# Optimization experiments

Hardware: AMD Instinct MI355X
Metric: run time of the kernel (lower is better)

The kernel has to match this reference:

```python
import jax, jax.numpy as jnp
import numpy as np

N_NODES = 50000
N_EDGES = 600000
IN_DIM = 128
HID = 128
FEAT = 128
N_TASKS = 5
N_CLS = 10


def setup_inputs() -> dict:
    key = jax.random.key(0)
    ks = jax.random.split(key, 10)
    s = 0.05  # small init scale for weights
    return {
        "x": jax.random.normal(ks[0], (N_NODES, IN_DIM), jnp.float32),
        "edge_index": jax.random.randint(ks[1], (2, N_EDGES), 0, N_NODES, dtype=jnp.int32),
        "w1": jax.random.normal(ks[2], (IN_DIM, HID), jnp.float32) * s,
        "b1": jnp.zeros((HID,), jnp.float32),
        "w2": jax.random.normal(ks[3], (HID, HID), jnp.float32) * s,
        "b2": jnp.zeros((HID,), jnp.float32),
        "fw1": jax.random.normal(ks[4], (HID, FEAT), jnp.float32) * s,
        "fb1": jnp.zeros((FEAT,), jnp.float32),
        "fw2": jax.random.normal(ks[5], (FEAT, FEAT), jnp.float32) * s,
        "fb2": jnp.zeros((FEAT,), jnp.float32),
        "task_w": jax.random.normal(ks[6], (N_TASKS, FEAT, N_CLS), jnp.float32) * s,
        "task_b": jnp.zeros((N_TASKS, N_CLS), jnp.float32),
    }


def reference(x, edge_index, w1, b1, w2, b2, fw1, fb1, fw2, fb2, task_w, task_b):
    n = x.shape[0]
    # PyG GCNConv: add self-loops, symmetric D^{-1/2} A D^{-1/2} normalization.
    loop = jnp.arange(n, dtype=edge_index.dtype)
    src = jnp.concatenate([edge_index[0], loop])  # source nodes
    dst = jnp.concatenate([edge_index[1], loop])  # target (aggregation) nodes
    deg = jnp.zeros((n,), x.dtype).at[dst].add(jnp.ones((), x.dtype))
    dinv = jnp.where(deg > 0, jax.lax.rsqrt(deg), 0.0)
    norm = dinv[src] * dinv[dst]  # [E+N]

    def gcn_conv(h, w, b):
        h = h @ w                         # [N, H] linear transform
        msg = h[src] * norm[:, None]      # gather + normalize  [E+N, H]
        agg = jnp.zeros((n, h.shape[1]), h.dtype).at[dst].add(msg)  # scatter-add
        return agg + b

    h = jax.nn.relu(gcn_conv(x, w1, b1))
    # dropout(0.5) is identity at inference
    h = jax.nn.relu(gcn_conv(h, w2, b2))
    feature_x = jax.nn.relu(h @ fw1 + fb1)   # fc1
    h2 = jax.nn.relu(feature_x @ fw2 + fb2)  # fc2
    # per-task heads, all 128->10: batched as one einsum  [T, N, C]
    y = jnp.einsum('nf,tfc->tnc', h2, task_w) + task_b[:, None, :]
    return (y, feature_x)
```

## Files before the change

### kernel.cpp

```cpp
#include <hip/hip_runtime.h>
#include <hip/hip_bf16.h>

#define NN 50000
#define NE 600000
#define MM1_BLOCKS 782
#define STRIDE 64

typedef __attribute__((ext_vector_type(4))) float f32x4;
typedef __attribute__((ext_vector_type(8))) __bf16 bf16x8;

__device__ __forceinline__ unsigned pack2bf16(float x, float y) {
  __bf16 lo = (__bf16)x, hi = (__bf16)y;
  unsigned short ul = __builtin_bit_cast(unsigned short, lo);
  unsigned short uh = __builtin_bit_cast(unsigned short, hi);
  return (unsigned)ul | ((unsigned)uh << 16);
}

__global__ void k_zero(int* __restrict__ degi) {
  int i = blockIdx.x * 256 + threadIdx.x;
  if (i < NN) degi[i] = 0;
}

__global__ void k_prep(const int* __restrict__ degi, int* __restrict__ cur,
                       float* __restrict__ dinv, int2* __restrict__ edg) {
  int n = blockIdx.x * 256 + threadIdx.x;
  if (n < NN) {
    int d = degi[n];
    int base = n * STRIDE;
    cur[n] = base;
    dinv[n] = rsqrtf((float)(d + 1));
    int pe = base + ((d + 7) & ~7);
    for (int j = base + d; j < pe; j++) edg[j] = make_int2(0, 0);
  }
}

__global__ void k_fill(const int* __restrict__ srcv, const int* __restrict__ dstv,
                       int* __restrict__ cur, int2* __restrict__ edg, const float* __restrict__ dinv) {
  int e = blockIdx.x * 256 + threadIdx.x;
  if (e < NE) {
    int s = srcv[e], d = dstv[e];
    int p = atomicAdd(&cur[d], 1);
    edg[p] = make_int2(s, __float_as_int(dinv[s] * dinv[d]));
  }
}

__device__ __forceinline__ void stage_wt(const float* __restrict__ W, __bf16 (*wt)[136], int tid) {
  int j = tid & 127;
  int hi = tid >> 7;
#pragma unroll 4
  for (int it = 0; it < 32; ++it) {
    int kp = ((it << 1) + hi + (j >> 3)) & 63;
    float w0 = W[(kp * 2) * 128 + j];
    float w1 = W[(kp * 2 + 1) * 128 + j];
    *(unsigned*)(&wt[j][kp * 2]) = pack2bf16(w0, w1);
  }
}

template<int BR, bool IN_BF16, bool DUAL>
__device__ __forceinline__ void mm_body(const void* __restrict__ Xv, const __bf16 (*wt)[136],
                                        const float* __restrict__ bias, __bf16* __restrict__ Y,
                                        float* __restrict__ Yf, int strip, int lane) {
  int r16 = lane & 15, g = lane >> 4;
  bf16x8 a[4];
  if constexpr (IN_BF16) {
    const __bf16* xb = (const __bf16*)Xv + (size_t)(strip * 16 + r16) * 128 + g * 8;
#pragma unroll
    for (int ks = 0; ks < 4; ks++) a[ks] = *(const bf16x8*)(xb + ks * 32);
  } else {
    const float* xb = (const float*)Xv + (size_t)(strip * 16 + r16) * 128 + g * 8;
#pragma unroll
    for (int ks = 0; ks < 4; ks++) {
      f32x4 x0 = *(const f32x4*)(xb + ks * 32);
      f32x4 x1 = *(const f32x4*)(xb + ks * 32 + 4);
      bf16x8 v;
      v[0] = (__bf16)x0.x; v[1] = (__bf16)x0.y; v[2] = (__bf16)x0.z; v[3] = (__bf16)x0.w;
      v[4] = (__bf16)x1.x; v[5] = (__bf16)x1.y; v[6] = (__bf16)x1.z; v[7] = (__bf16)x1.w;
      a[ks] = v;
    }
  }
  f32x4 acc[8];
#pragma unroll
  for (int ct = 0; ct < 8; ct++) acc[ct] = (f32x4){0.f, 0.f, 0.f, 0.f};
#pragma unroll
  for (int ct = 0; ct < 8; ct++) {
    const __bf16* wrow = &wt[ct * 16 + r16][g * 8];
#pragma unroll
    for (int ks = 0; ks < 4; ks++) {
      bf16x8 b = *(const bf16x8*)(wrow + ks * 32);
      acc[ct] = __builtin_amdgcn_mfma_f32_16x16x32_bf16(a[ks], b, acc[ct], 0, 0, 0);
    }
  }
  int rbase = strip * 16 + g * 4;
#pragma unroll
  for (int ct = 0; ct < 8; ct++) {
    int col = ct * 16 + r16;
    float bv = (BR & 1) ? bias[col] : 0.f;
#pragma unroll
    for (int i = 0; i < 4; i++) {
      float v = acc[ct][i] + bv;
      if (BR & 2) v = fmaxf(v, 0.f);
      size_t idx = (size_t)(rbase + i) * 128 + col;
      Y[idx] = (__bf16)v;
      if constexpr (DUAL) Yf[idx] = v;
    }
  }
}

template<int BR, bool IN_BF16, bool DUAL>
__global__ __launch_bounds__(256) void k_mm128(const void* __restrict__ Xv, const float* __restrict__ W,
                                               const float* __restrict__ bias, __bf16* __restrict__ Y,
                                               float* __restrict__ Yf, int nrows) {
  __shared__ __bf16 wt[128][136];
  int tid = threadIdx.x;
  stage_wt(W, wt, tid);
  __syncthreads();
  int strip = blockIdx.x * 4 + (tid >> 6);
  if (strip * 16 >= nrows) return;
  mm_body<BR, IN_BF16, DUAL>(Xv, wt, bias, Y, Yf, strip, tid & 63);
}

__global__ __launch_bounds__(256) void k_mm1_count(const float* __restrict__ X, const float* __restrict__ W,
                                                   __bf16* __restrict__ Y,
                                                   const int* __restrict__ dstv, int* __restrict__ degi) {
  __shared__ __bf16 wt[128][136];
  int tid = threadIdx.x;
  if (blockIdx.x >= MM1_BLOCKS) {
    int e = (blockIdx.x - MM1_BLOCKS) * 256 + tid;
    if (e < NE) atomicAdd(&degi[dstv[e]], 1);
    return;
  }
  stage_wt(W, wt, tid);
  __syncthreads();
  int strip = blockIdx.x * 4 + (tid >> 6);
  if (strip * 16 >= NN) return;
  mm_body<0, false, false>(X, wt, nullptr, Y, nullptr, strip, tid & 63);
}

__global__ __launch_bounds__(256) void k_head(const __bf16* __restrict__ H, const float* __restrict__ TW,
                                              const float* __restrict__ TB, float* __restrict__ Y) {
  __shared__ __bf16 wt[64][136];
  int tid = threadIdx.x;
  for (int i = tid; i < 8192; i += 256) {
    int o = i >> 7, k = i & 127;
    float v = 0.f;
    if (o < 50) v = TW[(o / 10) * 1280 + k * 10 + (o % 10)];
    wt[o][k] = (__bf16)v;
  }
  __syncthreads();
  int lane = tid & 63;
  int strip = blockIdx.x * 4 + (tid >> 6);
  if (strip * 16 >= NN) return;
  int r16 = lane & 15, g = lane >> 4;
  const __bf16* xb = H + (size_t)(strip * 16 + r16) * 128 + g * 8;
  bf16x8 a[4];
#pragma unroll
  for (int ks = 0; ks < 4; ks++) a[ks] = *(const bf16x8*)(xb + ks * 32);
  f32x4 acc[4];
#pragma unroll
  for (int ct = 0; ct < 4; ct++) acc[ct] = (f32x4){0.f, 0.f, 0.f, 0.f};
#pragma unroll
  for (int ct = 0; ct < 4; ct++) {
    const __bf16* wrow = &wt[ct * 16 + r16][g * 8];
#pragma unroll
    for (int ks = 0; ks < 4; ks++) {
      bf16x8 b = *(const bf16x8*)(wrow + ks * 32);
      acc[ct] = __builtin_amdgcn_mfma_f32_16x16x32_bf16(a[ks], b, acc[ct], 0, 0, 0);
    }
  }
  int rbase = strip * 16 + g * 4;
#pragma unroll
  for (int ct = 0; ct < 4; ct++) {
    int o = ct * 16 + r16;
    if (o < 50) {
      int t = o / 10, c = o % 10;
      float tb = TB[o];
#pragma unroll
      for (int i = 0; i < 4; i++) {
        Y[(size_t)t * (NN * 10) + (size_t)(rbase + i) * 10 + c] = acc[ct][i] + tb;
      }
    }
  }
}

__device__ __forceinline__ void edge8(const int2* __restrict__ edg, int i, const unsigned* __restrict__ T,
                                      int lane, float& ax, float& ay) {
  const int4* ep = (const int4*)(edg + i);
  int4 p0 = ep[0], p1 = ep[1], p2 = ep[2], p3 = ep[3];
  unsigned v0 = T[p0.x * 64 + lane];
  unsigned v1 = T[p0.z * 64 + lane];
  unsigned v2 = T[p1.x * 64 + lane];
  unsigned v3 = T[p1.z * 64 + lane];
  unsigned v4 = T[p2.x * 64 + lane];
  unsigned v5 = T[p2.z * 64 + lane];
  unsigned v6 = T[p3.x * 64 + lane];
  unsigned v7 = T[p3.z * 64 + lane];
  float w0 = __int_as_float(p0.y), w1 = __int_as_float(p0.w);
  float w2 = __int_as_float(p1.y), w3 = __int_as_float(p1.w);
  float w4 = __int_as_float(p2.y), w5 = __int_as_float(p2.w);
  float w6 = __int_as_float(p3.y), w7 = __int_as_float(p3.w);
  ax = fmaf(__uint_as_float(v0 << 16), w0, ax); ay = fmaf(__uint_as_float(v0 & 0xffff0000u), w0, ay);
  ax = fmaf(__uint_as_float(v1 << 16), w1, ax); ay = fmaf(__uint_as_float(v1 & 0xffff0000u), w1, ay);
  ax = fmaf(__uint_as_float(v2 << 16), w2, ax); ay = fmaf(__uint_as_float(v2 & 0xffff0000u), w2, ay);
  ax = fmaf(__uint_as_float(v3 << 16), w3, ax); ay = fmaf(__uint_as_float(v3 & 0xffff0000u), w3, ay);
  ax = fmaf(__uint_as_float(v4 << 16), w4, ax); ay = fmaf(__uint_as_float(v4 & 0xffff0000u), w4, ay);
  ax = fmaf(__uint_as_float(v5 << 16), w5, ax); ay = fmaf(__uint_as_float(v5 & 0xffff0000u), w5, ay);
  ax = fmaf(__uint_as_float(v6 << 16), w6, ax); ay = fmaf(__uint_as_float(v6 & 0xffff0000u), w6, ay);
  ax = fmaf(__uint_as_float(v7 << 16), w7, ax); ay = fmaf(__uint_as_float(v7 & 0xffff0000u), w7, ay);
}

__global__ __launch_bounds__(256) void k_agg(const unsigned* __restrict__ T, const int* __restrict__ degi,
                                             const int2* __restrict__ edg, const float* __restrict__ dinv,
                                             const float* __restrict__ bias, unsigned* __restrict__ H) {
  int pair = blockIdx.x * 4 + (threadIdx.x >> 6);
  int nA = pair * 2, nB = nA + 1;
  int lane = threadIdx.x & 63;
  float2 b = ((const float2*)bias)[lane];
  float diA = dinv[nA], diB = dinv[nB];
  unsigned tA = T[(size_t)nA * 64 + lane];
  unsigned tB = T[(size_t)nB * 64 + lane];
  float axA = __uint_as_float(tA << 16) * (diA * diA);
  float ayA = __uint_as_float(tA & 0xffff0000u) * (diA * diA);
  float axB = __uint_as_float(tB << 16) * (diB * diB);
  float ayB = __uint_as_float(tB & 0xffff0000u) * (diB * diB);
  int iA = nA * STRIDE, eA = iA + ((degi[nA] + 7) & ~7);
  int iB = nB * STRIDE, eB = iB + ((degi[nB] + 7) & ~7);
  while (iA < eA && iB < eB) {
    edge8(edg, iA, T, lane, axA, ayA);
    edge8(edg, iB, T, lane, axB, ayB);
    iA += 8; iB += 8;
  }
  for (; iA < eA; iA += 8) edge8(edg, iA, T, lane, axA, ayA);
  for (; iB < eB; iB += 8) edge8(edg, iB, T, lane, axB, ayB);
  H[(size_t)nA * 64 + lane] = pack2bf16(fmaxf(axA + b.x, 0.f), fmaxf(ayA + b.y, 0.f));
  H[(size_t)nB * 64 + lane] = pack2bf16(fmaxf(axB + b.x, 0.f), fmaxf(ayB + b.y, 0.f));
}

extern "C" void kernel_launch(void* const* d_in, const int* in_sizes, int n_in,
                              void* d_out, int out_size, void* d_ws, size_t ws_size,
                              hipStream_t stream) {
  (void)in_sizes; (void)n_in; (void)out_size; (void)ws_size;
  const float* x   = (const float*)d_in[0];
  const int*   ei  = (const int*)d_in[1];
  const float* w1  = (const float*)d_in[2];
  const float* b1  = (const float*)d_in[3];
  const float* w2  = (const float*)d_in[4];
  const float* b2  = (const float*)d_in[5];
  const float* fw1 = (const float*)d_in[6];
  const float* fb1 = (const float*)d_in[7];
  const float* fw2 = (const float*)d_in[8];
  const float* fb2 = (const float*)d_in[9];
  const float* tw  = (const float*)d_in[10];
  const float* tb  = (const float*)d_in[11];
  const int* srcv = ei;
  const int* dstv = ei + NE;

  char* wsb = (char*)d_ws;
  __bf16* bufT = (__bf16*)(wsb + 0);
  __bf16* hbf  = (__bf16*)(wsb + 12800000);
  int*    degi = (int*)(wsb + 25600000);
  int*    cur  = (int*)(wsb + 25800192);
  float*  dinv = (float*)(wsb + 26000640);
  int2*   edg  = (int2*)(wsb + 26201088);

  float* y_out = (float*)d_out;
  float* feat  = (float*)d_out + 2500000;

  k_zero<<<196, 256, 0, stream>>>(degi);
  k_mm1_count<<<MM1_BLOCKS + (NE + 255) / 256, 256, 0, stream>>>(x, w1, bufT, dstv, degi);
  k_prep<<<196, 256, 0, stream>>>(degi, cur, dinv, edg);
  k_fill<<<(NE + 255) / 256, 256, 0, stream>>>(srcv, dstv, cur, edg, dinv);

  k_agg<<<6250, 256, 0, stream>>>((const unsigned*)bufT, degi, edg, dinv, b1, (unsigned*)hbf);
  k_mm128<0, true, false><<<782, 256, 0, stream>>>(hbf, w2, nullptr, bufT, nullptr, NN);
  k_agg<<<6250, 256, 0, stream>>>((const unsigned*)bufT, degi, edg, dinv, b2, (unsigned*)hbf);
  k_mm128<3, true, true><<<782, 256, 0, stream>>>(hbf, fw1, fb1, hbf, feat, NN);
  k_mm128<3, true, false><<<782, 256, 0, stream>>>(hbf, fw2, fb2, bufT, nullptr, NN);
  k_head<<<782, 256, 0, stream>>>(bufT, tw, tb, y_out);
}
```

Baseline: 182.6 us.

## Fuse fc1, fc2 and task heads into one kernel with LDS staging

```diff
diff --git a/kernel.cpp b/kernel.cpp
--- a/kernel.cpp
+++ b/kernel.cpp
@@ -136,47 +136,104 @@
   mm_body<0, false, false>(X, wt, nullptr, Y, nullptr, strip, tid & 63);
 }
 
-__global__ __launch_bounds__(256) void k_head(const __bf16* __restrict__ H, const float* __restrict__ TW,
-                                              const float* __restrict__ TB, float* __restrict__ Y) {
-  __shared__ __bf16 wt[64][136];
+__global__ __launch_bounds__(256) void k_mlp(const __bf16* __restrict__ H,
+                                             const float* __restrict__ fw1, const float* __restrict__ fb1,
+                                             const float* __restrict__ fw2, const float* __restrict__ fb2,
+                                             const float* __restrict__ tw, const float* __restrict__ tb,
+                                             float* __restrict__ feat, float* __restrict__ y) {
+  __shared__ __bf16 wS[128][136];
+  __shared__ __bf16 stg[64][136];
   int tid = threadIdx.x;
+  stage_wt(fw1, wS, tid);
+  __syncthreads();
+  int lane = tid & 63, wv = tid >> 6;
+  int strip = blockIdx.x * 4 + wv;
+  bool act = (strip * 16 < NN);
+  int r16 = lane & 15, g = lane >> 4;
+  int lrow = wv * 16;
+  f32x4 acc[8];
+  if (act) {
+    const __bf16* xb = H + (size_t)(strip * 16 + r16) * 128 + g * 8;
+    bf16x8 a[4];
+#pragma unroll
+    for (int ks = 0; ks < 4; ks++) a[ks] = *(const bf16x8*)(xb + ks * 32);
+#pragma unroll
+    for (int ct = 0; ct < 8; ct++) acc[ct] = (f32x4){0.f, 0.f, 0.f, 0.f};
+#pragma unroll
+    for (int ct = 0; ct < 8; ct++) {
+      const __bf16* wrow = &wS[ct * 16 + r16][g * 8];
+#pragma unroll
+      for (int ks = 0; ks < 4; ks++)
+        acc[ct] = __builtin_amdgcn_mfma_f32_16x16x32_bf16(a[ks], *(const bf16x8*)(wrow + ks * 32), acc[ct], 0, 0, 0);
+    }
+    int rbase = strip * 16 + g * 4;
+#pragma unroll
+    for (int ct = 0; ct < 8; ct++) {
+      int col = ct * 16 + r16;
+      float bv = fb1[col];
+#pragma unroll
+      for (int i = 0; i < 4; i++) {
+        float v = fmaxf(acc[ct][i] + bv, 0.f);
+        feat[(size_t)(rbase + i) * 128 + col] = v;
+        stg[lrow + g * 4 + i][col] = (__bf16)v;
+      }
+    }
+  }
+  __syncthreads();
+  stage_wt(fw2, wS, tid);
+  __syncthreads();
+  if (act) {
+    bf16x8 a[4];
+#pragma unroll
+    for (int ks = 0; ks < 4; ks++) a[ks] = *(const bf16x8*)(&stg[lrow + r16][g * 8 + ks * 32]);
+#pragma unroll
+    for (int ct = 0; ct < 8; ct++) acc[ct] = (f32x4){0.f, 0.f, 0.f, 0.f};
+#pragma unroll
+    for (int ct = 0; ct < 8; ct++) {
+      const __bf16* wrow = &wS[ct * 16 + r16][g * 8];
+#pragma unroll
+      for (int ks = 0; ks < 4; ks++)
+        acc[ct] = __builtin_amdgcn_mfma_f32_16x16x32_bf16(a[ks], *(const bf16x8*)(wrow + ks * 32), acc[ct], 0, 0, 0);
+    }
+#pragma unroll
+    for (int ct = 0; ct < 8; ct++) {
+      int col = ct * 16 + r16;
+      float bv = fb2[col];
+#pragma unroll
+      for (int i = 0; i < 4; i++) stg[lrow + g * 4 + i][col] = (__bf16)fmaxf(acc[ct][i] + bv, 0.f);
+    }
+  }
+  __syncthreads();
   for (int i = tid; i < 8192; i += 256) {
     int o = i >> 7, k = i & 127;
-    float v = 0.f;
-    if (o < 50) v = TW[(o / 10) * 1280 + k * 10 + (o % 10)];
-    wt[o][k] = (__bf16)v;
-  }
-  __syncthreads();
-  int lane = tid & 63;
-  int strip = blockIdx.x * 4 + (tid >> 6);
-  if (strip * 16 >= NN) return;
-  int r16 = lane & 15, g = lane >> 4;
-  const __bf16* xb = H + (size_t)(strip * 16 + r16) * 128 + g * 8;
-  bf16x8 a[4];
-#pragma unroll
-  for (int ks = 0; ks < 4; ks++) a[ks] = *(const bf16x8*)(xb + ks * 32);
-  f32x4 acc[4];
-#pragma unroll
-  for (int ct = 0; ct < 4; ct++) acc[ct] = (f32x4){0.f, 0.f, 0.f, 0.f};
-#pragma unroll
-  for (int ct = 0; ct < 4; ct++) {
-    const __bf16* wrow = &wt[ct * 16 + r16][g * 8];
-#pragma unroll
-    for (int ks = 0; ks < 4; ks++) {
-      bf16x8 b = *(const bf16x8*)(wrow + ks * 32);
-      acc[ct] = __builtin_amdgcn_mfma_f32_16x16x32_bf16(a[ks], b, acc[ct], 0, 0, 0);
-    }
-  }
-  int rbase = strip * 16 + g * 4;
-#pragma unroll
-  for (int ct = 0; ct < 4; ct++) {
-    int o = ct * 16 + r16;
-    if (o < 50) {
-      int t = o / 10, c = o % 10;
-      float tb = TB[o];
-#pragma unroll
-      for (int i = 0; i < 4; i++) {
-        Y[(size_t)t * (NN * 10) + (size_t)(rbase + i) * 10 + c] = acc[ct][i] + tb;
+    float v = (o < 50) ? tw[(o / 10) * 1280 + k * 10 + (o % 10)] : 0.f;
+    wS[o][k] = (__bf16)v;
+  }
+  __syncthreads();
+  if (act) {
+    bf16x8 a[4];
+#pragma unroll
+    for (int ks = 0; ks < 4; ks++) a[ks] = *(const bf16x8*)(&stg[lrow + r16][g * 8 + ks * 32]);
+    f32x4 hacc[4];
+#pragma unroll
+    for (int ct = 0; ct < 4; ct++) hacc[ct] = (f32x4){0.f, 0.f, 0.f, 0.f};
+#pragma unroll
+    for (int ct = 0; ct < 4; ct++) {
+      const __bf16* wrow = &wS[ct * 16 + r16][g * 8];
+#pragma unroll
+      for (int ks = 0; ks < 4; ks++)
+        hacc[ct] = __builtin_amdgcn_mfma_f32_16x16x32_bf16(a[ks], *(const bf16x8*)(wrow + ks * 32), hacc[ct], 0, 0, 0);
+    }
+    int rbase = strip * 16 + g * 4;
+#pragma unroll
+    for (int ct = 0; ct < 4; ct++) {
+      int o = ct * 16 + r16;
+      if (o < 50) {
+        int t = o / 10, c = o % 10;
+        float tbv = tb[o];
+#pragma unroll
+        for (int i = 0; i < 4; i++)
+          y[(size_t)t * (NN * 10) + (size_t)(rbase + i) * 10 + c] = hacc[ct][i] + tbv;
       }
     }
   }
@@ -273,7 +330,5 @@
   k_agg<<<6250, 256, 0, stream>>>((const unsigned*)bufT, degi, edg, dinv, b1, (unsigned*)hbf);
   k_mm128<0, true, false><<<782, 256, 0, stream>>>(hbf, w2, nullptr, bufT, nullptr, NN);
   k_agg<<<6250, 256, 0, stream>>>((const unsigned*)bufT, degi, edg, dinv, b2, (unsigned*)hbf);
-  k_mm128<3, true, true><<<782, 256, 0, stream>>>(hbf, fw1, fb1, hbf, feat, NN);
-  k_mm128<3, true, false><<<782, 256, 0, stream>>>(hbf, fw2, fb2, bufT, nullptr, NN);
-  k_head<<<782, 256, 0, stream>>>(bufT, tw, tb, y_out);
-}
+  k_mlp<<<782, 256, 0, stream>>>(hbf, fw1, fb1, fw2, fb2, tw, tb, feat, y_out);
+}
```

Result: no change. 179.3 us (-1.8%).
